# Performance work log

Hardware: AMD Instinct MI355X
Metric: run time of the kernel (lower is better)

## Reference

```python
import jax, jax.numpy as jnp
import numpy as np

B, N, D = 4, 4096, 1024
STD = 1.0 / D

def setup_inputs() -> dict:
    key = jax.random.key(0)
    ks = jax.random.split(key, 6)
    return {
        "x_real": jax.random.normal(ks[0], (B, N, D), dtype=jnp.float32),
        "x_imag": jax.random.normal(ks[1], (B, N, D), dtype=jnp.float32),
        "w_query_real": jax.random.normal(ks[2], (D, D), dtype=jnp.float32) * STD,
        "w_query_imag": jax.random.normal(ks[3], (D, D), dtype=jnp.float32) * STD,
        "w_key": jax.random.normal(ks[4], (D, D), dtype=jnp.float32) * STD,
        "w_value": jax.random.normal(ks[5], (D, D), dtype=jnp.float32) * STD,
    }

def reference(x_real, x_imag, w_query_real, w_query_imag, w_key, w_value):
    # query gate: (x.real @ Wqr) * (x.imag @ Wqi)  -> [b, n, e]
    query = jnp.einsum('bnd,de->bne', x_real, w_query_real) * \
            jnp.einsum('bnd,de->bne', x_imag, w_query_imag)
    key = jnp.einsum('bnd,de->bne', x_real, w_key)      # [b, n, d]
    value = jnp.einsum('bnd,de->bne', x_imag, w_value)  # [b, n, e]
    # linear-attention style reduction over sequence dim n
    kv_attn = jnp.einsum('bnd,bne->bde', key, value)    # [b, d, e]
    # dropout with p=0.0 (eval / identity)
    bffn = jnp.einsum('bnd,bde->bne', query, kv_attn)   # [b, n, e]
    return bffn
```

## Files before the change

### kernel.cpp

```cpp
#include <hip/hip_runtime.h>
#include <stdint.h>

typedef unsigned short ushort_t;
typedef __attribute__((ext_vector_type(8))) short bf16x8;
typedef __attribute__((ext_vector_type(4))) float f32x4;

__device__ __forceinline__ ushort_t f2bf(float f) {
  union { float f; uint32_t u; } v; v.f = f;
  uint32_t u = v.u;
  u += 0x7FFFu + ((u >> 16) & 1u);
  return (ushort_t)(u >> 16);
}
__device__ __forceinline__ float bf2f(ushort_t h) {
  union { uint32_t u; float f; } v; v.u = ((uint32_t)h) << 16;
  return v.f;
}
__device__ __forceinline__ void gl2lds16(const void* g, void* l) {
  __builtin_amdgcn_global_load_lds(
      (__attribute__((address_space(1))) void*)(uintptr_t)g,
      (__attribute__((address_space(3))) void*)(uint32_t)(uintptr_t)l,
      16, 0, 0);
}

__device__ __forceinline__ void gemm_loop(
    const ushort_t* __restrict__ A, int lda,
    const ushort_t* __restrict__ Bt, int ldb,
    int m0, int n0, int K,
    ushort_t* __restrict__ As, ushort_t* __restrict__ Bs,
    f32x4 (&acc)[4][4]) {
  const int t = threadIdx.x;
  const int lane = t & 63, wid = t >> 6;
  const int wm = wid & 1, wn = wid >> 1;
  const int lr = lane & 15, lq = lane >> 4;

  const ushort_t* ap[4];
  const ushort_t* bp[4];
  int dst[4];
  #pragma unroll
  for (int i = 0; i < 4; ++i) {
    int slot = i * 256 + t;
    int row = slot >> 3, kgp = slot & 7;
    int kg = kgp ^ (row & 7);
    dst[i] = slot * 16;
    ap[i] = A + (size_t)(m0 + row) * lda + kg * 8;
    bp[i] = Bt + (size_t)(n0 + row) * ldb + kg * 8;
  }

  int aoff[2][4], boff[2][4];
  #pragma unroll
  for (int s = 0; s < 2; ++s)
    #pragma unroll
    for (int i = 0; i < 4; ++i) {
      int ra = wm * 64 + i * 16 + lr;
      aoff[s][i] = ra * 128 + (((s * 4 + lq) ^ (ra & 7)) * 16);
      int rb = wn * 64 + i * 16 + lr;
      boff[s][i] = rb * 128 + (((s * 4 + lq) ^ (rb & 7)) * 16);
    }

  for (int k0 = 0; k0 < K; k0 += 64) {
    #pragma unroll
    for (int i = 0; i < 4; ++i) gl2lds16(bp[i] + k0, (char*)Bs + dst[i]);
    #pragma unroll
    for (int i = 0; i < 4; ++i) gl2lds16(ap[i] + k0, (char*)As + dst[i]);
    __syncthreads();
    #pragma unroll
    for (int s = 0; s < 2; ++s) {
      bf16x8 af[4], bfr[4];
      #pragma unroll
      for (int i = 0; i < 4; ++i) af[i] = *(const bf16x8*)((const char*)As + aoff[s][i]);
      #pragma unroll
      for (int i = 0; i < 4; ++i) bfr[i] = *(const bf16x8*)((const char*)Bs + boff[s][i]);
      #pragma unroll
      for (int mi = 0; mi < 4; ++mi)
        #pragma unroll
        for (int ni = 0; ni < 4; ++ni)
          acc[mi][ni] = __builtin_amdgcn_mfma_f32_16x16x32_bf16(af[mi], bfr[ni], acc[mi][ni], 0, 0, 0);
    }
    __syncthreads();
  }
}

template <bool GATE>
__global__ __launch_bounds__(256) void proj_gemm(
    const ushort_t* __restrict__ X, const ushort_t* __restrict__ Wt,
    ushort_t* __restrict__ Cq, ushort_t* __restrict__ Ct,
    const ushort_t* __restrict__ gate) {
  __shared__ ushort_t smem[2 * 128 * 64];
  ushort_t* As = smem;
  ushort_t* Bs = smem + 128 * 64;
  const int bid = blockIdx.x;
  const int xcd = bid & 7, i = bid >> 3;
  const int m0 = (xcd * 16 + (i >> 4)) * 128;
  const int n0 = (i & 15) * 128;
  f32x4 acc[4][4] = {};
  gemm_loop(X, 1024, Wt, 1024, m0, n0, 1024, As, Bs, acc);

  const int t = threadIdx.x, lane = t & 63, wid = t >> 6;
  const int wm = wid & 1, wn = wid >> 1;
  const int lr = lane & 15, lq = lane >> 4;

  if (n0 < 1024) {
    #pragma unroll
    for (int mi = 0; mi < 4; ++mi) {
      int rbase = m0 + wm * 64 + mi * 16 + lq * 4;
      #pragma unroll
      for (int ni = 0; ni < 4; ++ni) {
        int c = n0 + wn * 64 + ni * 16 + lr;
        #pragma unroll
        for (int r = 0; r < 4; ++r) {
          float v = acc[mi][ni][r];
          if constexpr (GATE) v *= bf2f(gate[(size_t)(rbase + r) * 1024 + c]);
          Cq[(size_t)(rbase + r) * 1024 + c] = f2bf(v);
        }
      }
    }
  } else {
    #pragma unroll
    for (int mi = 0; mi < 4; ++mi) {
      int ns = wm * 64 + mi * 16 + lq * 4;
      int nc = ns >> 3, half = (ns >> 2) & 1;
      #pragma unroll
      for (int ni = 0; ni < 4; ++ni) {
        int dl = wn * 64 + ni * 16 + lr;
        ushort4 u = make_ushort4(f2bf(acc[mi][ni][0]), f2bf(acc[mi][ni][1]),
                                 f2bf(acc[mi][ni][2]), f2bf(acc[mi][ni][3]));
        *(ushort4*)((char*)smem + dl * 256 + ((nc ^ (dl & 15)) * 16) + half * 8) = u;
      }
    }
    __syncthreads();
    const int b = m0 >> 12, nseq0 = m0 & 4095;
    #pragma unroll
    for (int j = 0; j < 8; ++j) {
      int g = j * 256 + t;
      int dl = g >> 4, nc = g & 15;
      bf16x8 v = *(const bf16x8*)((const char*)smem + dl * 256 + ((nc ^ (dl & 15)) * 16));
      int d = n0 - 1024 + dl;
      *(bf16x8*)&Ct[(((size_t)(b * 1024 + d)) << 12) + nseq0 + nc * 8] = v;
    }
  }
}

__global__ __launch_bounds__(256) void kv_gemm(
    const ushort_t* __restrict__ VT, const ushort_t* __restrict__ KT,
    ushort_t* __restrict__ P) {
  __shared__ ushort_t smem[2 * 128 * 64];
  ushort_t* As = smem;
  ushort_t* Bs = smem + 128 * 64;
  const int bid = blockIdx.x;
  const int xcd = bid & 7, i = bid >> 3;
  const int z = xcd * 2 + (i >> 6);
  const int mn = i & 63;
  const int m0 = (mn >> 3) * 128, n0 = (mn & 7) * 128;
  const int b = z & 3, s = z >> 2;
  const ushort_t* A = VT + ((size_t)b << 22) + s * 1024;
  const ushort_t* Bt = KT + ((size_t)b << 22) + s * 1024;
  f32x4 acc[4][4] = {};
  gemm_loop(A, 4096, Bt, 4096, m0, n0, 1024, As, Bs, acc);

  const int t = threadIdx.x, lane = t & 63, wid = t >> 6;
  const int wm = wid & 1, wn = wid >> 1;
  const int lr = lane & 15, lq = lane >> 4;
  ushort_t* C = P + ((size_t)z << 20);
  #pragma unroll
  for (int mi = 0; mi < 4; ++mi) {
    int rbase = m0 + wm * 64 + mi * 16 + lq * 4;
    #pragma unroll
    for (int ni = 0; ni < 4; ++ni) {
      int c = n0 + wn * 64 + ni * 16 + lr;
      #pragma unroll
      for (int r = 0; r < 4; ++r)
        C[(size_t)(rbase + r) * 1024 + c] = f2bf(acc[mi][ni][r]);
    }
  }
}

__global__ __launch_bounds__(256) void kv_reduce(const ushort_t* __restrict__ P,
                                                 ushort_t* __restrict__ KVT) {
  size_t e4 = ((size_t)blockIdx.x * 256 + threadIdx.x) * 4;
  int b = (int)(e4 >> 20);
  size_t j = e4 & ((1u << 20) - 1);
  float s0 = 0.f, s1 = 0.f, s2 = 0.f, s3 = 0.f;
  #pragma unroll
  for (int sp = 0; sp < 4; ++sp) {
    ushort4 v = *(const ushort4*)(P + ((size_t)(sp * 4 + b) << 20) + j);
    s0 += bf2f(v.x); s1 += bf2f(v.y); s2 += bf2f(v.z); s3 += bf2f(v.w);
  }
  *(ushort4*)&KVT[e4] = make_ushort4(f2bf(s0), f2bf(s1), f2bf(s2), f2bf(s3));
}

__global__ __launch_bounds__(256) void fin_gemm(
    const ushort_t* __restrict__ Q, const ushort_t* __restrict__ KVT,
    float* __restrict__ Out) {
  __shared__ ushort_t smem[2 * 128 * 64];
  ushort_t* As = smem;
  ushort_t* Bs = smem + 128 * 64;
  const int bid = blockIdx.x;
  const int xcd = bid & 7, i = bid >> 3;
  const int m0 = (xcd * 16 + (i >> 3)) * 128;
  const int n0 = (i & 7) * 128;
  const int b = m0 >> 12;
  f32x4 acc[4][4] = {};
  gemm_loop(Q, 1024, KVT + ((size_t)b << 20), 1024, m0, n0, 1024, As, Bs, acc);

  const int t = threadIdx.x, lane = t & 63, wid = t >> 6;
  const int wm = wid & 1, wn = wid >> 1;
  const int lr = lane & 15, lq = lane >> 4;
  #pragma unroll
  for (int mi = 0; mi < 4; ++mi) {
    int rbase = m0 + wm * 64 + mi * 16 + lq * 4;
    #pragma unroll
    for (int ni = 0; ni < 4; ++ni) {
      int c = n0 + wn * 64 + ni * 16 + lr;
      #pragma unroll
      for (int r = 0; r < 4; ++r)
        Out[(size_t)(rbase + r) * 1024 + c] = acc[mi][ni][r];
    }
  }
}

__global__ __launch_bounds__(256) void prep(
    const float* __restrict__ xr, const float* __restrict__ xi,
    const float* w0, const float* w1, const float* w2, const float* w3,
    ushort_t* __restrict__ xrb, ushort_t* __restrict__ xib,
    ushort_t* o0, ushort_t* o1, ushort_t* o2, ushort_t* o3) {
  const int bid = blockIdx.x;
  const int t = threadIdx.x;
  if (bid < 4096) {
    __shared__ float tile[32][33];
    const float* W; ushort_t* O;
    switch (bid >> 10) {
      case 0: W = w0; O = o0; break;
      case 1: W = w1; O = o1; break;
      case 2: W = w2; O = o2; break;
      default: W = w3; O = o3; break;
    }
    const int within = bid & 1023;
    const int bx = (within & 31) * 32, by = (within >> 5) * 32;
    const int tx = t & 31, ty = t >> 5;
    #pragma unroll
    for (int k = 0; k < 32; k += 8)
      tile[ty + k][tx] = W[(size_t)(by + ty + k) * 1024 + bx + tx];
    __syncthreads();
    #pragma unroll
    for (int k = 0; k < 32; k += 8)
      O[(size_t)(bx + ty + k) * 1024 + by + tx] = f2bf(tile[tx][ty + k]);
  } else {
    const size_t T = 16u * 1024u * 1024u;
    size_t e = ((size_t)(bid - 4096) * 256 + t) * 8;
    const float* src; ushort_t* dst;
    if (e < T) { src = xr + e; dst = xrb + e; }
    else       { src = xi + (e - T); dst = xib + (e - T); }
    float4 f0 = *(const float4*)src;
    float4 f1 = *(const float4*)(src + 4);
    ushort4 u0 = make_ushort4(f2bf(f0.x), f2bf(f0.y), f2bf(f0.z), f2bf(f0.w));
    ushort4 u1 = make_ushort4(f2bf(f1.x), f2bf(f1.y), f2bf(f1.z), f2bf(f1.w));
    *(ushort4*)dst = u0;
    *(ushort4*)(dst + 4) = u1;
  }
}

extern "C" void kernel_launch(void* const* d_in, const int* in_sizes, int n_in,
                              void* d_out, int out_size, void* d_ws, size_t ws_size,
                              hipStream_t stream) {
  const float* xr  = (const float*)d_in[0];
  const float* xi  = (const float*)d_in[1];
  const float* wqr = (const float*)d_in[2];
  const float* wqi = (const float*)d_in[3];
  const float* wk  = (const float*)d_in[4];
  const float* wv  = (const float*)d_in[5];

  char* ws = (char*)d_ws;
  const size_t MB = 1024ull * 1024ull;
  ushort_t* WtQR = (ushort_t*)(ws + 0 * MB);
  ushort_t* WtK  = (ushort_t*)(ws + 2 * MB);
  ushort_t* WtQI = (ushort_t*)(ws + 4 * MB);
  ushort_t* WtV  = (ushort_t*)(ws + 6 * MB);
  ushort_t* Xrb  = (ushort_t*)(ws + 8 * MB);
  ushort_t* Xib  = (ushort_t*)(ws + 40 * MB);
  ushort_t* KT   = (ushort_t*)(ws + 72 * MB);
  ushort_t* Q    = (ushort_t*)(ws + 104 * MB);
  ushort_t* VT   = (ushort_t*)(ws + 8 * MB);
  ushort_t* KVT  = (ushort_t*)(ws + 40 * MB);
  ushort_t* QR   = (ushort_t*)d_out;
  ushort_t* KVP  = (ushort_t*)d_out;

  prep<<<20480, 256, 0, stream>>>(xr, xi, wqr, wqi, wk, wv,
                                  Xrb, Xib, WtQR, WtQI, WtK, WtV);
  proj_gemm<false><<<2048, 256, 0, stream>>>(Xrb, WtQR, QR, KT, nullptr);
  proj_gemm<true><<<2048, 256, 0, stream>>>(Xib, WtQI, Q, VT, QR);
  kv_gemm<<<1024, 256, 0, stream>>>(VT, KT, KVP);
  kv_reduce<<<4096, 256, 0, stream>>>(KVP, KVT);
  fin_gemm<<<1024, 256, 0, stream>>>(Q, KVT, (float*)d_out);
}
```

Baseline: 428.2 us.

## Switch GEMMs to 256x256 tiles with 8 waves and double-buffered LDS pipeline

Replaces the 128x128, 4-wave single-buffered GEMM main loop with a 256x256 tile computed by 8 waves. The new loop uses 128 KB of double-buffered dynamic LDS, interleaving global-to-LDS loads with MFMA groups and raising instruction priority around the MFMA bursts. The goal is to hide load latency and double operand reuse per tile. The cost is fewer blocks (256-512 per launch), so wave quantization and occupancy could suffer on 256 CUs, and register pressure rises with 32 accumulators per thread.

```diff
diff --git a/kernel.cpp b/kernel.cpp
--- a/kernel.cpp
+++ b/kernel.cpp
@@ -22,87 +22,138 @@
       16, 0, 0);
 }
 
-__device__ __forceinline__ void gemm_loop(
+__device__ __forceinline__ void gemm256(
     const ushort_t* __restrict__ A, int lda,
     const ushort_t* __restrict__ Bt, int ldb,
-    int m0, int n0, int K,
-    ushort_t* __restrict__ As, ushort_t* __restrict__ Bs,
-    f32x4 (&acc)[4][4]) {
+    int m0, int n0, int K, char* __restrict__ smem,
+    f32x4 (&acc)[8][4]) {
   const int t = threadIdx.x;
   const int lane = t & 63, wid = t >> 6;
-  const int wm = wid & 1, wn = wid >> 1;
+  const int wm = wid >> 2, wn = wid & 3;
   const int lr = lane & 15, lq = lane >> 4;
-
-  const ushort_t* ap[4];
-  const ushort_t* bp[4];
-  int dst[4];
-  #pragma unroll
-  for (int i = 0; i < 4; ++i) {
-    int slot = i * 256 + t;
-    int row = slot >> 3, kgp = slot & 7;
-    int kg = kgp ^ (row & 7);
-    dst[i] = slot * 16;
-    ap[i] = A + (size_t)(m0 + row) * lda + kg * 8;
-    bp[i] = Bt + (size_t)(n0 + row) * ldb + kg * 8;
-  }
-
-  int aoff[2][4], boff[2][4];
-  #pragma unroll
-  for (int s = 0; s < 2; ++s)
-    #pragma unroll
-    for (int i = 0; i < 4; ++i) {
-      int ra = wm * 64 + i * 16 + lr;
-      aoff[s][i] = ra * 128 + (((s * 4 + lq) ^ (ra & 7)) * 16);
-      int rb = wn * 64 + i * 16 + lr;
-      boff[s][i] = rb * 128 + (((s * 4 + lq) ^ (rb & 7)) * 16);
-    }
-
-  for (int k0 = 0; k0 < K; k0 += 64) {
-    #pragma unroll
-    for (int i = 0; i < 4; ++i) gl2lds16(bp[i] + k0, (char*)Bs + dst[i]);
-    #pragma unroll
-    for (int i = 0; i < 4; ++i) gl2lds16(ap[i] + k0, (char*)As + dst[i]);
-    __syncthreads();
-    #pragma unroll
-    for (int s = 0; s < 2; ++s) {
-      bf16x8 af[4], bfr[4];
-      #pragma unroll
-      for (int i = 0; i < 4; ++i) af[i] = *(const bf16x8*)((const char*)As + aoff[s][i]);
-      #pragma unroll
-      for (int i = 0; i < 4; ++i) bfr[i] = *(const bf16x8*)((const char*)Bs + boff[s][i]);
-      #pragma unroll
-      for (int mi = 0; mi < 4; ++mi)
-        #pragma unroll
-        for (int ni = 0; ni < 4; ++ni)
-          acc[mi][ni] = __builtin_amdgcn_mfma_f32_16x16x32_bf16(af[mi], bfr[ni], acc[mi][ni], 0, 0, 0);
-    }
-    __syncthreads();
-  }
+  const int nt = K >> 6;
+
+  const int row0 = t >> 3, row1 = (512 + t) >> 3;
+  const int kg0 = (t & 7) ^ (row0 & 7), kg1 = (t & 7) ^ (row1 & 7);
+  const ushort_t* a0 = A + (size_t)(m0 + row0) * lda + kg0 * 8;
+  const ushort_t* a1 = A + (size_t)(m0 + row1) * lda + kg1 * 8;
+  const ushort_t* b0 = Bt + (size_t)(n0 + row0) * ldb + kg0 * 8;
+  const ushort_t* b1 = Bt + (size_t)(n0 + row1) * ldb + kg1 * 8;
+  const int d0 = t * 16, d1 = (512 + t) * 16;
+
+  const int o0 = lr * 128 + ((lq ^ (lr & 7)) << 4);
+  const int o1 = lr * 128 + (((4 + lq) ^ (lr & 7)) << 4);
+  const char* aB = smem + wm * 16384;
+  const char* bB = smem + 65536 + wn * 8192;
+
+#define STG_A(tt, h, buf) do { if ((tt) < nt) { \
+    gl2lds16(a0 + (h) * 128 * lda + (tt) * 64, smem + (buf) * 32768 + (h) * 16384 + d0); \
+    gl2lds16(a1 + (h) * 128 * lda + (tt) * 64, smem + (buf) * 32768 + (h) * 16384 + d1); } } while (0)
+#define STG_B(tt, h, buf) do { if ((tt) < nt) { \
+    gl2lds16(b0 + (h) * 128 * ldb + (tt) * 64, smem + 65536 + (buf) * 32768 + (h) * 16384 + d0); \
+    gl2lds16(b1 + (h) * 128 * ldb + (tt) * 64, smem + 65536 + (buf) * 32768 + (h) * 16384 + d1); } } while (0)
+#define AF_(buf, mig, s) (*(const bf16x8*)(aB + (buf) * 32768 + (mig) * 2048 + o##s))
+#define BF_(buf, nig, s) (*(const bf16x8*)(bB + (buf) * 32768 + (nig) * 2048 + o##s))
+#define MFMA16(AR, M0, N0) \
+    __builtin_amdgcn_s_setprio(1); \
+    _Pragma("unroll") \
+    for (int mi = 0; mi < 4; ++mi) \
+      _Pragma("unroll") \
+      for (int ni = 0; ni < 2; ++ni) { \
+        acc[(M0) + mi][(N0) + ni] = __builtin_amdgcn_mfma_f32_16x16x32_bf16(AR[mi][0], bF[ni][0], acc[(M0) + mi][(N0) + ni], 0, 0, 0); \
+        acc[(M0) + mi][(N0) + ni] = __builtin_amdgcn_mfma_f32_16x16x32_bf16(AR[mi][1], bF[ni][1], acc[(M0) + mi][(N0) + ni], 0, 0, 0); \
+      } \
+    __builtin_amdgcn_s_setprio(0);
+
+  bf16x8 aLo[4][2], aHi[4][2], bF[2][2];
+
+  STG_A(0, 0, 0); STG_A(0, 1, 0); STG_B(0, 0, 0); STG_B(0, 1, 0);
+  STG_A(1, 0, 1); STG_A(1, 1, 1);
+  asm volatile("s_waitcnt vmcnt(4)" ::: "memory");
+  __builtin_amdgcn_s_barrier();
+
+  const int niter = nt >> 1;
+  for (int i = 0; i < niter; ++i) {
+    const int t2 = 2 * i + 2, t3 = 2 * i + 3;
+    #pragma unroll
+    for (int mi = 0; mi < 4; ++mi) { aLo[mi][0] = AF_(0, mi, 0); aLo[mi][1] = AF_(0, mi, 1); }
+    #pragma unroll
+    for (int ni = 0; ni < 2; ++ni) { bF[ni][0] = BF_(0, ni, 0); bF[ni][1] = BF_(0, ni, 1); }
+    STG_B(2 * i + 1, 0, 1);
+    __builtin_amdgcn_s_barrier();
+    MFMA16(aLo, 0, 0)
+    __builtin_amdgcn_s_barrier();
+    #pragma unroll
+    for (int mi = 0; mi < 4; ++mi) { aHi[mi][0] = AF_(0, 4 + mi, 0); aHi[mi][1] = AF_(0, 4 + mi, 1); }
+    STG_B(2 * i + 1, 1, 1);
+    __builtin_amdgcn_s_barrier();
+    MFMA16(aHi, 4, 0)
+    __builtin_amdgcn_s_barrier();
+    #pragma unroll
+    for (int ni = 0; ni < 2; ++ni) { bF[ni][0] = BF_(0, 2 + ni, 0); bF[ni][1] = BF_(0, 2 + ni, 1); }
+    STG_A(t2, 0, 0);
+    __builtin_amdgcn_s_barrier();
+    MFMA16(aLo, 0, 2)
+    __builtin_amdgcn_s_barrier();
+    STG_A(t2, 1, 0);
+    __builtin_amdgcn_s_barrier();
+    MFMA16(aHi, 4, 2)
+    asm volatile("s_waitcnt vmcnt(4)" ::: "memory");
+    __builtin_amdgcn_s_barrier();
+    #pragma unroll
+    for (int mi = 0; mi < 4; ++mi) { aLo[mi][0] = AF_(1, mi, 0); aLo[mi][1] = AF_(1, mi, 1); }
+    #pragma unroll
+    for (int ni = 0; ni < 2; ++ni) { bF[ni][0] = BF_(1, ni, 0); bF[ni][1] = BF_(1, ni, 1); }
+    STG_B(t2, 0, 0);
+    __builtin_amdgcn_s_barrier();
+    MFMA16(aLo, 0, 0)
+    __builtin_amdgcn_s_barrier();
+    #pragma unroll
+    for (int mi = 0; mi < 4; ++mi) { aHi[mi][0] = AF_(1, 4 + mi, 0); aHi[mi][1] = AF_(1, 4 + mi, 1); }
+    STG_B(t2, 1, 0);
+    __builtin_amdgcn_s_barrier();
+    MFMA16(aHi, 4, 0)
+    __builtin_amdgcn_s_barrier();
+    #pragma unroll
+    for (int ni = 0; ni < 2; ++ni) { bF[ni][0] = BF_(1, 2 + ni, 0); bF[ni][1] = BF_(1, 2 + ni, 1); }
+    STG_A(t3, 0, 1);
+    __builtin_amdgcn_s_barrier();
+    MFMA16(aLo, 0, 2)
+    __builtin_amdgcn_s_barrier();
+    STG_A(t3, 1, 1);
+    __builtin_amdgcn_s_barrier();
+    MFMA16(aHi, 4, 2)
+    asm volatile("s_waitcnt vmcnt(4)" ::: "memory");
+    __builtin_amdgcn_s_barrier();
+  }
+#undef STG_A
+#undef STG_B
+#undef AF_
+#undef BF_
+#undef MFMA16
 }
 
 template <bool GATE>
-__global__ __launch_bounds__(256) void proj_gemm(
+__global__ __launch_bounds__(512, 2) void proj8(
     const ushort_t* __restrict__ X, const ushort_t* __restrict__ Wt,
     ushort_t* __restrict__ Cq, ushort_t* __restrict__ Ct,
     const ushort_t* __restrict__ gate) {
-  __shared__ ushort_t smem[2 * 128 * 64];
-  ushort_t* As = smem;
-  ushort_t* Bs = smem + 128 * 64;
+  extern __shared__ char smem[];
   const int bid = blockIdx.x;
   const int xcd = bid & 7, i = bid >> 3;
-  const int m0 = (xcd * 16 + (i >> 4)) * 128;
-  const int n0 = (i & 15) * 128;
-  f32x4 acc[4][4] = {};
-  gemm_loop(X, 1024, Wt, 1024, m0, n0, 1024, As, Bs, acc);
+  const int m0 = (xcd * 8 + (i >> 3)) * 256;
+  const int n0 = (i & 7) * 256;
+  f32x4 acc[8][4] = {};
+  gemm256(X, 1024, Wt, 1024, m0, n0, 1024, smem, acc);
 
   const int t = threadIdx.x, lane = t & 63, wid = t >> 6;
-  const int wm = wid & 1, wn = wid >> 1;
+  const int wm = wid >> 2, wn = wid & 3;
   const int lr = lane & 15, lq = lane >> 4;
 
   if (n0 < 1024) {
     #pragma unroll
-    for (int mi = 0; mi < 4; ++mi) {
-      int rbase = m0 + wm * 64 + mi * 16 + lq * 4;
+    for (int mi = 0; mi < 8; ++mi) {
+      int rbase = m0 + wm * 128 + mi * 16 + lq * 4;
       #pragma unroll
       for (int ni = 0; ni < 4; ++ni) {
         int c = n0 + wn * 64 + ni * 16 + lr;
@@ -115,55 +166,54 @@
       }
     }
   } else {
-    #pragma unroll
-    for (int mi = 0; mi < 4; ++mi) {
-      int ns = wm * 64 + mi * 16 + lq * 4;
-      int nc = ns >> 3, half = (ns >> 2) & 1;
+    __syncthreads();
+    #pragma unroll
+    for (int mi = 0; mi < 8; ++mi) {
+      int ns0 = wm * 128 + mi * 16 + lq * 4;
+      int nc = ns0 >> 3, half8 = (ns0 >> 2) & 1;
       #pragma unroll
       for (int ni = 0; ni < 4; ++ni) {
         int dl = wn * 64 + ni * 16 + lr;
         ushort4 u = make_ushort4(f2bf(acc[mi][ni][0]), f2bf(acc[mi][ni][1]),
                                  f2bf(acc[mi][ni][2]), f2bf(acc[mi][ni][3]));
-        *(ushort4*)((char*)smem + dl * 256 + ((nc ^ (dl & 15)) * 16) + half * 8) = u;
+        *(ushort4*)(smem + dl * 512 + ((nc ^ (dl & 31)) * 16) + half8 * 8) = u;
       }
     }
     __syncthreads();
     const int b = m0 >> 12, nseq0 = m0 & 4095;
     #pragma unroll
-    for (int j = 0; j < 8; ++j) {
-      int g = j * 256 + t;
-      int dl = g >> 4, nc = g & 15;
-      bf16x8 v = *(const bf16x8*)((const char*)smem + dl * 256 + ((nc ^ (dl & 15)) * 16));
+    for (int j = 0; j < 16; ++j) {
+      int g = j * 512 + t;
+      int dl = g >> 5, nc = g & 31;
+      bf16x8 v = *(const bf16x8*)(smem + dl * 512 + ((nc ^ (dl & 31)) * 16));
       int d = n0 - 1024 + dl;
       *(bf16x8*)&Ct[(((size_t)(b * 1024 + d)) << 12) + nseq0 + nc * 8] = v;
     }
   }
 }
 
-__global__ __launch_bounds__(256) void kv_gemm(
+__global__ __launch_bounds__(512, 2) void kv8(
     const ushort_t* __restrict__ VT, const ushort_t* __restrict__ KT,
     ushort_t* __restrict__ P) {
-  __shared__ ushort_t smem[2 * 128 * 64];
-  ushort_t* As = smem;
-  ushort_t* Bs = smem + 128 * 64;
+  extern __shared__ char smem[];
   const int bid = blockIdx.x;
   const int xcd = bid & 7, i = bid >> 3;
-  const int z = xcd * 2 + (i >> 6);
-  const int mn = i & 63;
-  const int m0 = (mn >> 3) * 128, n0 = (mn & 7) * 128;
+  const int z = xcd * 2 + (i >> 4);
+  const int mn = i & 15;
+  const int m0 = (mn >> 2) * 256, n0 = (mn & 3) * 256;
   const int b = z & 3, s = z >> 2;
   const ushort_t* A = VT + ((size_t)b << 22) + s * 1024;
   const ushort_t* Bt = KT + ((size_t)b << 22) + s * 1024;
-  f32x4 acc[4][4] = {};
-  gemm_loop(A, 4096, Bt, 4096, m0, n0, 1024, As, Bs, acc);
+  f32x4 acc[8][4] = {};
+  gemm256(A, 4096, Bt, 4096, m0, n0, 1024, smem, acc);
 
   const int t = threadIdx.x, lane = t & 63, wid = t >> 6;
-  const int wm = wid & 1, wn = wid >> 1;
+  const int wm = wid >> 2, wn = wid & 3;
   const int lr = lane & 15, lq = lane >> 4;
   ushort_t* C = P + ((size_t)z << 20);
   #pragma unroll
-  for (int mi = 0; mi < 4; ++mi) {
-    int rbase = m0 + wm * 64 + mi * 16 + lq * 4;
+  for (int mi = 0; mi < 8; ++mi) {
+    int rbase = m0 + wm * 128 + mi * 16 + lq * 4;
     #pragma unroll
     for (int ni = 0; ni < 4; ++ni) {
       int c = n0 + wn * 64 + ni * 16 + lr;
@@ -188,26 +238,24 @@
   *(ushort4*)&KVT[e4] = make_ushort4(f2bf(s0), f2bf(s1), f2bf(s2), f2bf(s3));
 }
 
-__global__ __launch_bounds__(256) void fin_gemm(
+__global__ __launch_bounds__(512, 2) void fin8(
     const ushort_t* __restrict__ Q, const ushort_t* __restrict__ KVT,
     float* __restrict__ Out) {
-  __shared__ ushort_t smem[2 * 128 * 64];
-  ushort_t* As = smem;
-  ushort_t* Bs = smem + 128 * 64;
+  extern __shared__ char smem[];
   const int bid = blockIdx.x;
   const int xcd = bid & 7, i = bid >> 3;
-  const int m0 = (xcd * 16 + (i >> 3)) * 128;
-  const int n0 = (i & 7) * 128;
+  const int m0 = (xcd * 8 + (i >> 2)) * 256;
+  const int n0 = (i & 3) * 256;
   const int b = m0 >> 12;
-  f32x4 acc[4][4] = {};
-  gemm_loop(Q, 1024, KVT + ((size_t)b << 20), 1024, m0, n0, 1024, As, Bs, acc);
+  f32x4 acc[8][4] = {};
+  gemm256(Q, 1024, KVT + ((size_t)b << 20), 1024, m0, n0, 1024, smem, acc);
 
   const int t = threadIdx.x, lane = t & 63, wid = t >> 6;
-  const int wm = wid & 1, wn = wid >> 1;
+  const int wm = wid >> 2, wn = wid & 3;
   const int lr = lane & 15, lq = lane >> 4;
   #pragma unroll
-  for (int mi = 0; mi < 4; ++mi) {
-    int rbase = m0 + wm * 64 + mi * 16 + lq * 4;
+  for (int mi = 0; mi < 8; ++mi) {
+    int rbase = m0 + wm * 128 + mi * 16 + lq * 4;
     #pragma unroll
     for (int ni = 0; ni < 4; ++ni) {
       int c = n0 + wn * 64 + ni * 16 + lr;
@@ -284,11 +332,20 @@
   ushort_t* QR   = (ushort_t*)d_out;
   ushort_t* KVP  = (ushort_t*)d_out;
 
+  static bool inited = false;
+  if (!inited) {
+    inited = true;
+    hipFuncSetAttribute((const void*)&proj8<false>, hipFuncAttributeMaxDynamicSharedMemorySize, 131072);
+    hipFuncSetAttribute((const void*)&proj8<true>,  hipFuncAttributeMaxDynamicSharedMemorySize, 131072);
+    hipFuncSetAttribute((const void*)&kv8,          hipFuncAttributeMaxDynamicSharedMemorySize, 131072);
+    hipFuncSetAttribute((const void*)&fin8,         hipFuncAttributeMaxDynamicSharedMemorySize, 131072);
+  }
+
   prep<<<20480, 256, 0, stream>>>(xr, xi, wqr, wqi, wk, wv,
                                   Xrb, Xib, WtQR, WtQI, WtK, WtV);
-  proj_gemm<false><<<2048, 256, 0, stream>>>(Xrb, WtQR, QR, KT, nullptr);
-  proj_gemm<true><<<2048, 256, 0, stream>>>(Xib, WtQI, Q, VT, QR);
-  kv_gemm<<<1024, 256, 0, stream>>>(VT, KT, KVP);
+  proj8<false><<<512, 512, 131072, stream>>>(Xrb, WtQR, QR, KT, nullptr);
+  proj8<true><<<512, 512, 131072, stream>>>(Xib, WtQI, Q, VT, QR);
+  kv8<<<256, 512, 131072, stream>>>(VT, KT, KVP);
   kv_reduce<<<4096, 256, 0, stream>>>(KVP, KVT);
-  fin_gemm<<<1024, 256, 0, stream>>>(Q, KVT, (float*)d_out);
-}
+  fin8<<<256, 512, 131072, stream>>>(Q, KVT, (float*)d_out);
+}
```

Measured after the change: 402.6 us. 1.06x faster.

## Switch GEMMs to 256x128 tiles with 8 waves and double-buffered LDS

Applied to the files above, without the earlier changes.

Replaces the shared 128x128, 4-wave GEMM loop with a 256x128 tile run by 8 waves. The K step drops to 32 and the loop double-buffers global-to-LDS loads, so it needs only one barrier per iteration, and MFMA sections are raised in priority with setprio. This aims to hide load latency and halve the number of barriers. In exchange it uses 48KB of dynamic LDS per block and needs a reworked two-pass transposed epilogue. All projection, kv and final kernels are relaunched with half as many blocks.

```diff
diff --git a/kernel.cpp b/kernel.cpp
--- a/kernel.cpp
+++ b/kernel.cpp
@@ -22,81 +22,75 @@
       16, 0, 0);
 }
 
-__device__ __forceinline__ void gemm_loop(
+__device__ __forceinline__ void gemm256x128(
     const ushort_t* __restrict__ A, int lda,
     const ushort_t* __restrict__ Bt, int ldb,
-    int m0, int n0, int K,
-    ushort_t* __restrict__ As, ushort_t* __restrict__ Bs,
+    int m0, int n0, int K, char* __restrict__ smem,
     f32x4 (&acc)[4][4]) {
   const int t = threadIdx.x;
   const int lane = t & 63, wid = t >> 6;
-  const int wm = wid & 1, wn = wid >> 1;
-  const int lr = lane & 15, lq = lane >> 4;
-
-  const ushort_t* ap[4];
-  const ushort_t* bp[4];
-  int dst[4];
-  #pragma unroll
-  for (int i = 0; i < 4; ++i) {
-    int slot = i * 256 + t;
-    int row = slot >> 3, kgp = slot & 7;
-    int kg = kgp ^ (row & 7);
-    dst[i] = slot * 16;
-    ap[i] = A + (size_t)(m0 + row) * lda + kg * 8;
-    bp[i] = Bt + (size_t)(n0 + row) * ldb + kg * 8;
-  }
-
-  int aoff[2][4], boff[2][4];
-  #pragma unroll
-  for (int s = 0; s < 2; ++s)
-    #pragma unroll
-    for (int i = 0; i < 4; ++i) {
-      int ra = wm * 64 + i * 16 + lr;
-      aoff[s][i] = ra * 128 + (((s * 4 + lq) ^ (ra & 7)) * 16);
-      int rb = wn * 64 + i * 16 + lr;
-      boff[s][i] = rb * 128 + (((s * 4 + lq) ^ (rb & 7)) * 16);
-    }
-
-  for (int k0 = 0; k0 < K; k0 += 64) {
-    #pragma unroll
-    for (int i = 0; i < 4; ++i) gl2lds16(bp[i] + k0, (char*)Bs + dst[i]);
-    #pragma unroll
-    for (int i = 0; i < 4; ++i) gl2lds16(ap[i] + k0, (char*)As + dst[i]);
-    __syncthreads();
-    #pragma unroll
-    for (int s = 0; s < 2; ++s) {
-      bf16x8 af[4], bfr[4];
-      #pragma unroll
-      for (int i = 0; i < 4; ++i) af[i] = *(const bf16x8*)((const char*)As + aoff[s][i]);
-      #pragma unroll
-      for (int i = 0; i < 4; ++i) bfr[i] = *(const bf16x8*)((const char*)Bs + boff[s][i]);
-      #pragma unroll
-      for (int mi = 0; mi < 4; ++mi)
-        #pragma unroll
-        for (int ni = 0; ni < 4; ++ni)
-          acc[mi][ni] = __builtin_amdgcn_mfma_f32_16x16x32_bf16(af[mi], bfr[ni], acc[mi][ni], 0, 0, 0);
-    }
-    __syncthreads();
-  }
+  const int wm = wid >> 1, wn = wid & 1;
+  const int lr = lane & 15, lq = lane >> 4;
+  const int nt = K >> 5;
+
+  const int rowS = t >> 2;
+  const int kgS = (t & 3) ^ (rowS & 3);
+  const ushort_t* a0 = A + (size_t)(m0 + rowS) * lda + kgS * 8;
+  const ushort_t* a1 = a0 + (size_t)128 * lda;
+  const ushort_t* b0 = Bt + (size_t)(n0 + rowS) * ldb + kgS * 8;
+  const int d0 = t * 16;
+
+  const int o = lr * 64 + ((lq ^ (lr & 3)) << 4);
+  const int aW = wm * 4096;
+  const int bW = 16384 + wn * 4096;
+
+#define STAGE(tt, buf) do { \
+    char* s = smem + (buf); \
+    gl2lds16(a0 + (tt) * 32, s + d0); \
+    gl2lds16(a1 + (tt) * 32, s + 8192 + d0); \
+    gl2lds16(b0 + (tt) * 32, s + 16384 + d0); \
+  } while (0)
+
+  bf16x8 aF[4], bF[4];
+
+  STAGE(0, 0);
+  for (int tt = 0; tt < nt; ++tt) {
+    asm volatile("s_waitcnt vmcnt(0) lgkmcnt(0)\n\ts_barrier" ::: "memory");
+    const int cb = (tt & 1) ? 24576 : 0;
+    if (tt + 1 < nt) STAGE(tt + 1, (tt & 1) ? 0 : 24576);
+    const char* base = smem + cb;
+    #pragma unroll
+    for (int mi = 0; mi < 4; ++mi)
+      aF[mi] = *(const bf16x8*)(base + aW + mi * 1024 + o);
+    #pragma unroll
+    for (int ni = 0; ni < 4; ++ni)
+      bF[ni] = *(const bf16x8*)(base + bW + ni * 1024 + o);
+    __builtin_amdgcn_s_setprio(1);
+    #pragma unroll
+    for (int mi = 0; mi < 4; ++mi)
+      #pragma unroll
+      for (int ni = 0; ni < 4; ++ni)
+        acc[mi][ni] = __builtin_amdgcn_mfma_f32_16x16x32_bf16(aF[mi], bF[ni], acc[mi][ni], 0, 0, 0);
+    __builtin_amdgcn_s_setprio(0);
+  }
+#undef STAGE
 }
 
 template <bool GATE>
-__global__ __launch_bounds__(256) void proj_gemm(
+__global__ __launch_bounds__(512, 4) void proj8(
     const ushort_t* __restrict__ X, const ushort_t* __restrict__ Wt,
     ushort_t* __restrict__ Cq, ushort_t* __restrict__ Ct,
     const ushort_t* __restrict__ gate) {
-  __shared__ ushort_t smem[2 * 128 * 64];
-  ushort_t* As = smem;
-  ushort_t* Bs = smem + 128 * 64;
+  extern __shared__ char smem[];
   const int bid = blockIdx.x;
   const int xcd = bid & 7, i = bid >> 3;
-  const int m0 = (xcd * 16 + (i >> 4)) * 128;
+  const int m0 = (xcd * 8 + (i >> 4)) * 256;
   const int n0 = (i & 15) * 128;
   f32x4 acc[4][4] = {};
-  gemm_loop(X, 1024, Wt, 1024, m0, n0, 1024, As, Bs, acc);
+  gemm256x128(X, 1024, Wt, 1024, m0, n0, 1024, smem, acc);
 
   const int t = threadIdx.x, lane = t & 63, wid = t >> 6;
-  const int wm = wid & 1, wn = wid >> 1;
+  const int wm = wid >> 1, wn = wid & 1;
   const int lr = lane & 15, lq = lane >> 4;
 
   if (n0 < 1024) {
@@ -115,50 +109,53 @@
       }
     }
   } else {
-    #pragma unroll
-    for (int mi = 0; mi < 4; ++mi) {
-      int ns = wm * 64 + mi * 16 + lq * 4;
-      int nc = ns >> 3, half = (ns >> 2) & 1;
-      #pragma unroll
-      for (int ni = 0; ni < 4; ++ni) {
-        int dl = wn * 64 + ni * 16 + lr;
-        ushort4 u = make_ushort4(f2bf(acc[mi][ni][0]), f2bf(acc[mi][ni][1]),
-                                 f2bf(acc[mi][ni][2]), f2bf(acc[mi][ni][3]));
-        *(ushort4*)((char*)smem + dl * 256 + ((nc ^ (dl & 15)) * 16) + half * 8) = u;
+    const int b = m0 >> 12, nseq0 = m0 & 4095;
+    #pragma unroll
+    for (int p = 0; p < 2; ++p) {
+      __syncthreads();
+      #pragma unroll
+      for (int mi = 0; mi < 4; ++mi) {
+        int ns0 = wm * 64 + mi * 16 + lq * 4;
+        int nc = ns0 >> 3, half8 = (ns0 >> 2) & 1;
+        #pragma unroll
+        for (int nib = 0; nib < 2; ++nib) {
+          int ni = p * 2 + nib;
+          int row = wn * 32 + nib * 16 + lr;
+          ushort4 u = make_ushort4(f2bf(acc[mi][ni][0]), f2bf(acc[mi][ni][1]),
+                                   f2bf(acc[mi][ni][2]), f2bf(acc[mi][ni][3]));
+          *(ushort4*)(smem + row * 512 + ((nc ^ (row & 31)) * 16) + half8 * 8) = u;
+        }
       }
-    }
-    __syncthreads();
-    const int b = m0 >> 12, nseq0 = m0 & 4095;
-    #pragma unroll
-    for (int j = 0; j < 8; ++j) {
-      int g = j * 256 + t;
-      int dl = g >> 4, nc = g & 15;
-      bf16x8 v = *(const bf16x8*)((const char*)smem + dl * 256 + ((nc ^ (dl & 15)) * 16));
-      int d = n0 - 1024 + dl;
-      *(bf16x8*)&Ct[(((size_t)(b * 1024 + d)) << 12) + nseq0 + nc * 8] = v;
-    }
-  }
-}
-
-__global__ __launch_bounds__(256) void kv_gemm(
+      __syncthreads();
+      #pragma unroll
+      for (int j = 0; j < 4; ++j) {
+        int g = j * 512 + t;
+        int r = g >> 5, nc2 = g & 31;
+        bf16x8 v = *(const bf16x8*)(smem + r * 512 + ((nc2 ^ (r & 31)) * 16));
+        int d = n0 - 1024 + (r >> 5) * 64 + p * 32 + ((r >> 4) & 1) * 16 + (r & 15);
+        *(bf16x8*)&Ct[(((size_t)(b * 1024 + d)) << 12) + nseq0 + nc2 * 8] = v;
+      }
+    }
+  }
+}
+
+__global__ __launch_bounds__(512, 4) void kv8(
     const ushort_t* __restrict__ VT, const ushort_t* __restrict__ KT,
     ushort_t* __restrict__ P) {
-  __shared__ ushort_t smem[2 * 128 * 64];
-  ushort_t* As = smem;
-  ushort_t* Bs = smem + 128 * 64;
+  extern __shared__ char smem[];
   const int bid = blockIdx.x;
   const int xcd = bid & 7, i = bid >> 3;
-  const int z = xcd * 2 + (i >> 6);
-  const int mn = i & 63;
-  const int m0 = (mn >> 3) * 128, n0 = (mn & 7) * 128;
+  const int z = xcd * 2 + (i >> 5);
+  const int mn = i & 31;
+  const int m0 = (mn >> 3) * 256, n0 = (mn & 7) * 128;
   const int b = z & 3, s = z >> 2;
   const ushort_t* A = VT + ((size_t)b << 22) + s * 1024;
   const ushort_t* Bt = KT + ((size_t)b << 22) + s * 1024;
   f32x4 acc[4][4] = {};
-  gemm_loop(A, 4096, Bt, 4096, m0, n0, 1024, As, Bs, acc);
+  gemm256x128(A, 4096, Bt, 4096, m0, n0, 1024, smem, acc);
 
   const int t = threadIdx.x, lane = t & 63, wid = t >> 6;
-  const int wm = wid & 1, wn = wid >> 1;
+  const int wm = wid >> 1, wn = wid & 1;
   const int lr = lane & 15, lq = lane >> 4;
   ushort_t* C = P + ((size_t)z << 20);
   #pragma unroll
@@ -188,22 +185,20 @@
   *(ushort4*)&KVT[e4] = make_ushort4(f2bf(s0), f2bf(s1), f2bf(s2), f2bf(s3));
 }
 
-__global__ __launch_bounds__(256) void fin_gemm(
+__global__ __launch_bounds__(512, 4) void fin8(
     const ushort_t* __restrict__ Q, const ushort_t* __restrict__ KVT,
     float* __restrict__ Out) {
-  __shared__ ushort_t smem[2 * 128 * 64];
-  ushort_t* As = smem;
-  ushort_t* Bs = smem + 128 * 64;
+  extern __shared__ char smem[];
   const int bid = blockIdx.x;
   const int xcd = bid & 7, i = bid >> 3;
-  const int m0 = (xcd * 16 + (i >> 3)) * 128;
+  const int m0 = (xcd * 8 + (i >> 3)) * 256;
   const int n0 = (i & 7) * 128;
   const int b = m0 >> 12;
   f32x4 acc[4][4] = {};
-  gemm_loop(Q, 1024, KVT + ((size_t)b << 20), 1024, m0, n0, 1024, As, Bs, acc);
+  gemm256x128(Q, 1024, KVT + ((size_t)b << 20), 1024, m0, n0, 1024, smem, acc);
 
   const int t = threadIdx.x, lane = t & 63, wid = t >> 6;
-  const int wm = wid & 1, wn = wid >> 1;
+  const int wm = wid >> 1, wn = wid & 1;
   const int lr = lane & 15, lq = lane >> 4;
   #pragma unroll
   for (int mi = 0; mi < 4; ++mi) {
@@ -284,11 +279,20 @@
   ushort_t* QR   = (ushort_t*)d_out;
   ushort_t* KVP  = (ushort_t*)d_out;
 
+  static bool inited = false;
+  if (!inited) {
+    inited = true;
+    hipFuncSetAttribute((const void*)&proj8<false>, hipFuncAttributeMaxDynamicSharedMemorySize, 49152);
+    hipFuncSetAttribute((const void*)&proj8<true>,  hipFuncAttributeMaxDynamicSharedMemorySize, 49152);
+    hipFuncSetAttribute((const void*)&kv8,          hipFuncAttributeMaxDynamicSharedMemorySize, 49152);
+    hipFuncSetAttribute((const void*)&fin8,         hipFuncAttributeMaxDynamicSharedMemorySize, 49152);
+  }
+
   prep<<<20480, 256, 0, stream>>>(xr, xi, wqr, wqi, wk, wv,
                                   Xrb, Xib, WtQR, WtQI, WtK, WtV);
-  proj_gemm<false><<<2048, 256, 0, stream>>>(Xrb, WtQR, QR, KT, nullptr);
-  proj_gemm<true><<<2048, 256, 0, stream>>>(Xib, WtQI, Q, VT, QR);
-  kv_gemm<<<1024, 256, 0, stream>>>(VT, KT, KVP);
+  proj8<false><<<1024, 512, 49152, stream>>>(Xrb, WtQR, QR, KT, nullptr);
+  proj8<true><<<1024, 512, 49152, stream>>>(Xib, WtQI, Q, VT, QR);
+  kv8<<<512, 512, 49152, stream>>>(VT, KT, KVP);
   kv_reduce<<<4096, 256, 0, stream>>>(KVP, KVT);
-  fin_gemm<<<1024, 256, 0, stream>>>(Q, KVT, (float*)d_out);
-}
+  fin8<<<512, 512, 49152, stream>>>(Q, KVT, (float*)d_out);
+}
```

New measurement: 420.9 us. About the same (-1.7%).
